# Kernel optimization log

Hardware: AMD Instinct MI355X
Metric: run time of the kernel (lower is better)

Reference implementation:

```python
import jax, jax.numpy as jnp
import numpy as np

B, S, D = 4, 2048, 1024
E = 8          # num_experts
K = 2          # top-k
H = 2048       # expert_dim


def setup_inputs() -> dict:
    key = jax.random.key(0)
    ks = jax.random.split(key, 7)
    sd = 1.0 / np.sqrt(D)
    sh = 1.0 / np.sqrt(H)
    return {
        "x": jax.random.normal(ks[0], (B, S, D), dtype=jnp.float32),
        "gate_w": jax.random.uniform(ks[1], (D, E), jnp.float32, -sd, sd),
        "gate_b": jax.random.uniform(ks[2], (E,), jnp.float32, -sd, sd),
        "w1": jax.random.uniform(ks[3], (E, D, H), jnp.float32, -sd, sd),
        "b1": jax.random.uniform(ks[4], (E, H), jnp.float32, -sd, sd),
        "w2": jax.random.uniform(ks[5], (E, H, D), jnp.float32, -sh, sh),
        "b2": jax.random.uniform(ks[6], (E, D), jnp.float32, -sh, sh),
    }


def reference(x, gate_w, gate_b, w1, b1, w2, b2):
    T = B * S
    x_flat = x.reshape(T, D)
    # gating
    gate_probs = jax.nn.softmax(x_flat @ gate_w + gate_b, axis=-1)  # [T, E]
    topw, topi = jax.lax.top_k(gate_probs, K)                        # [T, K]
    topw = topw / (jnp.sum(topw, axis=-1, keepdims=True) + 1e-9)
    # dense combine weights [T, E] (top-k indices are unique per token)
    combine = jnp.zeros((T, E), x.dtype).at[jnp.arange(T)[:, None], topi].add(topw)
    # all-experts FFN: relu(x @ W1 + b1) @ W2 + b2 per expert
    h = jax.nn.relu(jnp.einsum('td,edh->eth', x_flat, w1) + b1[:, None, :])  # [E, T, H]
    y = jnp.einsum('eth,ehd->etd', h, w2) + b2[:, None, :]                    # [E, T, D]
    out = jnp.einsum('etd,te->td', y, combine)
    return out.reshape(B, S, D)
```

## Files before the change

### kernel.cpp

```cpp
#include <hip/hip_runtime.h>
#include <hip/hip_bf16.h>
#include <math.h>

#define T_TOK 8192
#define D_DIM 1024
#define E_NUM 8
#define H_DIM 2048

typedef __bf16 bf16;
typedef __bf16 bf16x8 __attribute__((ext_vector_type(8)));
typedef __bf16 bf16x4 __attribute__((ext_vector_type(4)));
typedef float  f32x4  __attribute__((ext_vector_type(4)));

__device__ __forceinline__ void gload_lds16(const void* g, void* s) {
    __builtin_amdgcn_global_load_lds(
        (const __attribute__((address_space(1))) unsigned int*)g,
        (__attribute__((address_space(3))) unsigned int*)s, 16, 0, 0);
}

__global__ void cvt_x_kernel(const float* __restrict__ x, bf16* __restrict__ xb) {
    int i = blockIdx.x * blockDim.x + threadIdx.x;
    const float4* xp = (const float4*)x;
    float4 a = xp[i * 2];
    float4 b = xp[i * 2 + 1];
    bf16x8 o;
    o[0] = (bf16)a.x; o[1] = (bf16)a.y; o[2] = (bf16)a.z; o[3] = (bf16)a.w;
    o[4] = (bf16)b.x; o[5] = (bf16)b.y; o[6] = (bf16)b.z; o[7] = (bf16)b.w;
    *(bf16x8*)(xb + (size_t)i * 8) = o;
}

template <int K, int N>
__global__ void transpose_kernel(const float* __restrict__ W, bf16* __restrict__ Wt) {
    const int e  = blockIdx.z;
    const int kb = blockIdx.y * 32;
    const int nb = blockIdx.x * 32;
    __shared__ float tile[32][33];
    const float* We  = W  + (size_t)e * K * N;
    bf16*        Wte = Wt + (size_t)e * N * K;
    const int tid = threadIdx.x;
    const int r  = tid >> 3;
    const int c4 = (tid & 7) * 4;
    float4 v = *(const float4*)(We + (size_t)(kb + r) * N + nb + c4);
    tile[r][c4 + 0] = v.x; tile[r][c4 + 1] = v.y;
    tile[r][c4 + 2] = v.z; tile[r][c4 + 3] = v.w;
    __syncthreads();
    const int rn = tid >> 3;
    const int k4 = (tid & 7) * 4;
    bf16x4 o;
    o[0] = (bf16)tile[k4 + 0][rn]; o[1] = (bf16)tile[k4 + 1][rn];
    o[2] = (bf16)tile[k4 + 2][rn]; o[3] = (bf16)tile[k4 + 3][rn];
    *(bf16x4*)(Wte + (size_t)(nb + rn) * K + kb + k4) = o;
}

__global__ __launch_bounds__(256) void gating_kernel(
    const float* __restrict__ x, const float* __restrict__ gw,
    const float* __restrict__ gb,
    int* __restrict__ eIdx, float* __restrict__ wgt) {
    __shared__ float xs[4 * D_DIM];
    const int tid  = threadIdx.x;
    const int wave = tid >> 6;
    const int lane = tid & 63;
    {
        const float4* src = (const float4*)(x + (size_t)blockIdx.x * 4 * D_DIM);
        float4* dst = (float4*)xs;
#pragma unroll
        for (int k = 0; k < 4; k++) dst[tid + k * 256] = src[tid + k * 256];
    }
    __syncthreads();

    const int e = lane & 7;
    const int s = lane >> 3;
    const float* xw = xs + wave * D_DIM;
    double acc_a = 0.0, acc_b = 0.0;
#pragma unroll 8
    for (int i = 0; i < 128; i += 2) {
        int d0 = i * 8 + s;
        int d1 = (i + 1) * 8 + s;
        acc_a += (double)xw[d0] * (double)gw[d0 * 8 + e];
        acc_b += (double)xw[d1] * (double)gw[d1 * 8 + e];
    }
    double acc = acc_a + acc_b;
    acc += __shfl_xor(acc, 8, 64);
    acc += __shfl_xor(acc, 16, 64);
    acc += __shfl_xor(acc, 32, 64);
    double lg[E_NUM];
#pragma unroll
    for (int k = 0; k < E_NUM; k++) lg[k] = __shfl(acc, k, 64);

    if (lane == 0) {
        int token = blockIdx.x * 4 + wave;
        double v[E_NUM], p[E_NUM];
        double mx = -1e300;
#pragma unroll
        for (int k = 0; k < E_NUM; k++) { v[k] = lg[k] + (double)gb[k]; mx = fmax(mx, v[k]); }
        double sum = 0.0;
#pragma unroll
        for (int k = 0; k < E_NUM; k++) { p[k] = exp(v[k] - mx); sum += p[k]; }
        int i0 = 0; double p0 = p[0];
#pragma unroll
        for (int k = 1; k < E_NUM; k++) if (p[k] > p0) { p0 = p[k]; i0 = k; }
        int i1 = -1; double p1 = -1.0;
#pragma unroll
        for (int k = 0; k < E_NUM; k++) if (k != i0 && p[k] > p1) { p1 = p[k]; i1 = k; }
        double q0 = p0 / sum, q1 = p1 / sum;
        double sw = q0 + q1 + 1e-9;
        eIdx[token * 2]     = i0;
        eIdx[token * 2 + 1] = i1;
        wgt[token * 2]      = (float)(q0 / sw);
        wgt[token * 2 + 1]  = (float)(q1 / sw);
    }
}

__global__ void count_kernel(const int* __restrict__ eIdx, int* __restrict__ counts) {
    __shared__ int bc[E_NUM];
    const int tid = threadIdx.x;
    if (tid < E_NUM) bc[tid] = 0;
    __syncthreads();
    int2 ev = *(const int2*)(eIdx + (size_t)blockIdx.x * 512 + tid * 2);
    atomicAdd(&bc[ev.x], 1);
    atomicAdd(&bc[ev.y], 1);
    __syncthreads();
    if (tid < E_NUM) atomicAdd(&counts[tid], bc[tid]);
}

__global__ void scan_kernel(const int* __restrict__ counts, int* __restrict__ offsets) {
    if (threadIdx.x == 0) {
        int s = 0;
        for (int e = 0; e < E_NUM; e++) { offsets[e] = s; s += counts[e]; }
    }
}

__global__ void scatter_kernel(const int* __restrict__ eIdx, const int* __restrict__ offsets,
                               const float* __restrict__ wgt, int* __restrict__ fill,
                               int* __restrict__ rowIdx, float* __restrict__ wslot) {
    __shared__ int bc[E_NUM];
    __shared__ int bbase[E_NUM];
    __shared__ int bcur[E_NUM];
    const int tid = threadIdx.x;
    if (tid < E_NUM) { bc[tid] = 0; bcur[tid] = 0; }
    __syncthreads();
    int t0 = blockIdx.x * 512 + tid * 2;
    int4 ev = *(const int4*)(eIdx + (size_t)t0 * 2);
    float4 wv = *(const float4*)(wgt + (size_t)t0 * 2);
    atomicAdd(&bc[ev.x], 1);
    atomicAdd(&bc[ev.y], 1);
    atomicAdd(&bc[ev.z], 1);
    atomicAdd(&bc[ev.w], 1);
    __syncthreads();
    if (tid < E_NUM) bbase[tid] = atomicAdd(&fill[tid], bc[tid]);
    __syncthreads();
    int p0 = atomicAdd(&bcur[ev.x], 1);
    int r0 = offsets[ev.x] + bbase[ev.x] + p0;
    rowIdx[r0] = t0;     wslot[r0] = wv.x;
    int p1 = atomicAdd(&bcur[ev.y], 1);
    int r1 = offsets[ev.y] + bbase[ev.y] + p1;
    rowIdx[r1] = t0;     wslot[r1] = wv.y;
    int p2 = atomicAdd(&bcur[ev.z], 1);
    int r2 = offsets[ev.z] + bbase[ev.z] + p2;
    rowIdx[r2] = t0 + 1; wslot[r2] = wv.z;
    int p3 = atomicAdd(&bcur[ev.w], 1);
    int r3 = offsets[ev.w] + bbase[ev.w] + p3;
    rowIdx[r3] = t0 + 1; wslot[r3] = wv.w;
}

template <int KD, int ND, bool RELU, bool GATHER, bool COMBINE>
__global__ __launch_bounds__(256, 2) void moe_gemm_kernel(
    const bf16* __restrict__ A, const bf16* __restrict__ Bt,
    const float* __restrict__ bias, bf16* __restrict__ Out,
    const int* __restrict__ counts, const int* __restrict__ offsets,
    const int* __restrict__ rowIdx, const float* __restrict__ wslot,
    float* __restrict__ outF) {
    const int e  = blockIdx.z;
    const int Ne = counts[e];
    const int rb = blockIdx.y;
    if (rb * 128 >= Ne) return;
    const int base = offsets[e];
    const int n0   = blockIdx.x * 128;
    const bf16*  Be = Bt + (size_t)e * KD * ND;
    const float* be = bias + (size_t)e * ND;

    __shared__ bf16 As[128 * 64];
    __shared__ bf16 Bs[128 * 64];

    const int tid  = threadIdx.x;
    const int wave = tid >> 6;
    const int lane = tid & 63;

    const int sr = lane >> 3;
    const int cg = (lane & 7) ^ sr;
    const bf16* aP[4];
    const bf16* bP[4];
#pragma unroll
    for (int i = 0; i < 4; i++) {
        int m = rb * 128 + i * 32 + wave * 8 + sr;
        if (m >= Ne) m = Ne - 1;
        int arow = GATHER ? rowIdx[base + m] : (base + m);
        aP[i] = A + (size_t)arow * KD + cg * 8;
        int n = n0 + i * 32 + wave * 8 + sr;
        bP[i] = Be + (size_t)n * KD + cg * 8;
    }

    const int wm = (wave >> 1) * 64;
    const int wn = (wave & 1) * 64;
    const int lrow = lane & 15;
    const int quad = lane >> 4;
    const int r7   = lrow & 7;

    f32x4 acc[4][4] = {};

    for (int k0 = 0; k0 < KD; k0 += 64) {
#pragma unroll
        for (int i = 0; i < 4; i++) {
            gload_lds16(aP[i] + k0, (char*)As + i * 4096 + wave * 1024);
            gload_lds16(bP[i] + k0, (char*)Bs + i * 4096 + wave * 1024);
        }
        __syncthreads();

#pragma unroll
        for (int h = 0; h < 2; h++) {
            bf16x8 af[4], bfv[4];
#pragma unroll
            for (int t4 = 0; t4 < 4; t4++) {
                int pc = (quad + h * 4) ^ r7;
                af[t4]  = *(const bf16x8*)&As[(wm + t4 * 16 + lrow) * 64 + pc * 8];
                bfv[t4] = *(const bf16x8*)&Bs[(wn + t4 * 16 + lrow) * 64 + pc * 8];
            }
#pragma unroll
            for (int ti = 0; ti < 4; ti++)
#pragma unroll
                for (int tj = 0; tj < 4; tj++)
                    acc[ti][tj] = __builtin_amdgcn_mfma_f32_16x16x32_bf16(
                        af[ti], bfv[tj], acc[ti][tj], 0, 0, 0);
        }
        __syncthreads();
    }

    int   tokr[4][4];
    float wr[4][4];
    if (COMBINE) {
#pragma unroll
        for (int ti = 0; ti < 4; ti++)
#pragma unroll
            for (int r = 0; r < 4; r++) {
                int grow = rb * 128 + wm + ti * 16 + quad * 4 + r;
                if (grow < Ne) {
                    tokr[ti][r] = rowIdx[base + grow];
                    wr[ti][r]   = wslot[base + grow];
                }
            }
    }
#pragma unroll
    for (int ti = 0; ti < 4; ti++) {
        int rloc = wm + ti * 16 + quad * 4;
#pragma unroll
        for (int tj = 0; tj < 4; tj++) {
            int gcol = n0 + wn + tj * 16 + lrow;
            float bb = be[gcol];
#pragma unroll
            for (int r = 0; r < 4; r++) {
                int grow = rb * 128 + rloc + r;
                if (grow < Ne) {
                    float v = acc[ti][tj][r] + bb;
                    if (RELU) v = v > 0.f ? v : 0.f;
                    if (COMBINE) {
                        atomicAdd(&outF[(size_t)tokr[ti][r] * ND + gcol], v * wr[ti][r]);
                    } else {
                        Out[(size_t)(base + grow) * ND + gcol] = (bf16)v;
                    }
                }
            }
        }
    }
}

extern "C" void kernel_launch(void* const* d_in, const int* in_sizes, int n_in,
                              void* d_out, int out_size, void* d_ws, size_t ws_size,
                              hipStream_t stream) {
    const float* x  = (const float*)d_in[0];
    const float* gw = (const float*)d_in[1];
    const float* gb = (const float*)d_in[2];
    const float* w1 = (const float*)d_in[3];
    const float* b1 = (const float*)d_in[4];
    const float* w2 = (const float*)d_in[5];
    const float* b2 = (const float*)d_in[6];
    float* out = (float*)d_out;

    char* ws = (char*)d_ws;
    int*   counts = (int*)ws;
    int*   fill   = (int*)(ws + 32);
    int*   offs   = (int*)(ws + 64);
    int*   eIdx   = (int*)(ws + 256);
    float* wgt    = (float*)(ws + 65792);
    float* wslot  = (float*)(ws + 131328);
    int*   rowIdx = (int*)(ws + 196864);
    bf16*  Xb  = (bf16*)(ws + 262400);
    bf16*  Hb  = (bf16*)(ws + 17039616);
    bf16*  W2t = (bf16*)(ws + 84148480);
    bf16*  W1t = (bf16*)(ws + 117702912);

    if (ws_size < (size_t)151257344) return;

    hipMemsetAsync(ws, 0, 64, stream);
    hipMemsetAsync(out, 0, (size_t)T_TOK * D_DIM * 4, stream);
    cvt_x_kernel<<<(T_TOK * D_DIM) / (256 * 8), 256, 0, stream>>>(x, Xb);
    transpose_kernel<D_DIM, H_DIM>
        <<<dim3(H_DIM / 32, D_DIM / 32, E_NUM), 256, 0, stream>>>(w1, W1t);
    transpose_kernel<H_DIM, D_DIM>
        <<<dim3(D_DIM / 32, H_DIM / 32, E_NUM), 256, 0, stream>>>(w2, W2t);
    gating_kernel<<<T_TOK / 4, 256, 0, stream>>>(x, gw, gb, eIdx, wgt);
    count_kernel<<<T_TOK * 2 / 512, 256, 0, stream>>>(eIdx, counts);
    scan_kernel<<<1, 64, 0, stream>>>(counts, offs);
    scatter_kernel<<<T_TOK / 512, 256, 0, stream>>>(eIdx, offs, wgt, fill, rowIdx, wslot);
    moe_gemm_kernel<D_DIM, H_DIM, true, true, false>
        <<<dim3(H_DIM / 128, T_TOK / 128, E_NUM), 256, 0, stream>>>(
            Xb, W1t, b1, Hb, counts, offs, rowIdx, (const float*)nullptr, (float*)nullptr);
    moe_gemm_kernel<H_DIM, D_DIM, false, false, true>
        <<<dim3(D_DIM / 128, T_TOK / 128, E_NUM), 256, 0, stream>>>(
            Hb, W2t, b2, (bf16*)nullptr, counts, offs, rowIdx, wslot, out);
}
```

Measured before the change: 477.2 us.

## Double-buffer MoE GEMM K-loop and fuse x bf16 conversion into gating

Reworks the MoE GEMM main loop to use a 32-wide K step with two LDS buffers, so global-to-LDS loads for the next step are issued before computing on the current one and only one barrier is needed per iteration. The swizzle and loader mapping change to fit the narrower tile. It also removes the separate x-to-bf16 conversion kernel and has the gating kernel write the bf16 copy from its shared-memory tile, saving one launch and one read of x. The risks are more iterations with fewer MFMAs each and possible LDS bank conflicts from the new swizzle.

```diff
diff --git a/kernel.cpp b/kernel.cpp
--- a/kernel.cpp
+++ b/kernel.cpp
@@ -16,17 +16,6 @@
     __builtin_amdgcn_global_load_lds(
         (const __attribute__((address_space(1))) unsigned int*)g,
         (__attribute__((address_space(3))) unsigned int*)s, 16, 0, 0);
-}
-
-__global__ void cvt_x_kernel(const float* __restrict__ x, bf16* __restrict__ xb) {
-    int i = blockIdx.x * blockDim.x + threadIdx.x;
-    const float4* xp = (const float4*)x;
-    float4 a = xp[i * 2];
-    float4 b = xp[i * 2 + 1];
-    bf16x8 o;
-    o[0] = (bf16)a.x; o[1] = (bf16)a.y; o[2] = (bf16)a.z; o[3] = (bf16)a.w;
-    o[4] = (bf16)b.x; o[5] = (bf16)b.y; o[6] = (bf16)b.z; o[7] = (bf16)b.w;
-    *(bf16x8*)(xb + (size_t)i * 8) = o;
 }
 
 template <int K, int N>
@@ -55,7 +44,7 @@
 __global__ __launch_bounds__(256) void gating_kernel(
     const float* __restrict__ x, const float* __restrict__ gw,
     const float* __restrict__ gb,
-    int* __restrict__ eIdx, float* __restrict__ wgt) {
+    int* __restrict__ eIdx, float* __restrict__ wgt, bf16* __restrict__ xb) {
     __shared__ float xs[4 * D_DIM];
     const int tid  = threadIdx.x;
     const int wave = tid >> 6;
@@ -67,6 +56,17 @@
         for (int k = 0; k < 4; k++) dst[tid + k * 256] = src[tid + k * 256];
     }
     __syncthreads();
+
+    {
+        const int i0 = tid * 16;
+        bf16x8 o0, o1;
+#pragma unroll
+        for (int i = 0; i < 8; i++) o0[i] = (bf16)xs[i0 + i];
+#pragma unroll
+        for (int i = 0; i < 8; i++) o1[i] = (bf16)xs[i0 + 8 + i];
+        *(bf16x8*)(xb + (size_t)blockIdx.x * 4096 + i0)     = o0;
+        *(bf16x8*)(xb + (size_t)blockIdx.x * 4096 + i0 + 8) = o1;
+    }
 
     const int e = lane & 7;
     const int s = lane >> 3;
@@ -179,60 +179,66 @@
     const bf16*  Be = Bt + (size_t)e * KD * ND;
     const float* be = bias + (size_t)e * ND;
 
-    __shared__ bf16 As[128 * 64];
-    __shared__ bf16 Bs[128 * 64];
+    __shared__ bf16 SL[2 * 8192];
 
     const int tid  = threadIdx.x;
     const int wave = tid >> 6;
     const int lane = tid & 63;
 
-    const int sr = lane >> 3;
-    const int cg = (lane & 7) ^ sr;
-    const bf16* aP[4];
-    const bf16* bP[4];
-#pragma unroll
-    for (int i = 0; i < 4; i++) {
-        int m = rb * 128 + i * 32 + wave * 8 + sr;
+    const int srow = tid >> 2;
+    const int cg   = (tid & 3) ^ ((tid >> 3) & 3);
+    const bf16* aP[2];
+    const bf16* bP[2];
+#pragma unroll
+    for (int j = 0; j < 2; j++) {
+        int m = rb * 128 + j * 64 + srow;
         if (m >= Ne) m = Ne - 1;
         int arow = GATHER ? rowIdx[base + m] : (base + m);
-        aP[i] = A + (size_t)arow * KD + cg * 8;
-        int n = n0 + i * 32 + wave * 8 + sr;
-        bP[i] = Be + (size_t)n * KD + cg * 8;
-    }
-
-    const int wm = (wave >> 1) * 64;
-    const int wn = (wave & 1) * 64;
+        aP[j] = A + (size_t)arow * KD + cg * 8;
+        int n = n0 + j * 64 + srow;
+        bP[j] = Be + (size_t)n * KD + cg * 8;
+    }
+
+    const int wm   = (wave >> 1) * 64;
+    const int wn   = (wave & 1) * 64;
     const int lrow = lane & 15;
     const int quad = lane >> 4;
-    const int r7   = lrow & 7;
+    const int pc   = quad ^ ((lrow >> 1) & 3);
 
     f32x4 acc[4][4] = {};
 
-    for (int k0 = 0; k0 < KD; k0 += 64) {
-#pragma unroll
-        for (int i = 0; i < 4; i++) {
-            gload_lds16(aP[i] + k0, (char*)As + i * 4096 + wave * 1024);
-            gload_lds16(bP[i] + k0, (char*)Bs + i * 4096 + wave * 1024);
+    const int nit = KD / 32;
+#pragma unroll
+    for (int j = 0; j < 2; j++) {
+        gload_lds16(aP[j], (char*)SL + j * 4096 + wave * 1024);
+        gload_lds16(bP[j], (char*)SL + 8192 + j * 4096 + wave * 1024);
+    }
+    for (int it = 0; it < nit; it++) {
+        __syncthreads();
+        const int cb = it & 1;
+        if (it + 1 < nit) {
+            const int k1 = (it + 1) * 32;
+            char* dst = (char*)SL + (cb ^ 1) * 16384;
+#pragma unroll
+            for (int j = 0; j < 2; j++) {
+                gload_lds16(aP[j] + k1, dst + j * 4096 + wave * 1024);
+                gload_lds16(bP[j] + k1, dst + 8192 + j * 4096 + wave * 1024);
+            }
         }
-        __syncthreads();
-
-#pragma unroll
-        for (int h = 0; h < 2; h++) {
-            bf16x8 af[4], bfv[4];
-#pragma unroll
-            for (int t4 = 0; t4 < 4; t4++) {
-                int pc = (quad + h * 4) ^ r7;
-                af[t4]  = *(const bf16x8*)&As[(wm + t4 * 16 + lrow) * 64 + pc * 8];
-                bfv[t4] = *(const bf16x8*)&Bs[(wn + t4 * 16 + lrow) * 64 + pc * 8];
-            }
-#pragma unroll
-            for (int ti = 0; ti < 4; ti++)
-#pragma unroll
-                for (int tj = 0; tj < 4; tj++)
-                    acc[ti][tj] = __builtin_amdgcn_mfma_f32_16x16x32_bf16(
-                        af[ti], bfv[tj], acc[ti][tj], 0, 0, 0);
+        const bf16* As = SL + cb * 8192;
+        const bf16* Bs = As + 4096;
+        bf16x8 af[4], bfv[4];
+#pragma unroll
+        for (int t4 = 0; t4 < 4; t4++) {
+            af[t4]  = *(const bf16x8*)&As[(wm + t4 * 16 + lrow) * 32 + pc * 8];
+            bfv[t4] = *(const bf16x8*)&Bs[(wn + t4 * 16 + lrow) * 32 + pc * 8];
         }
-        __syncthreads();
+#pragma unroll
+        for (int ti = 0; ti < 4; ti++)
+#pragma unroll
+            for (int tj = 0; tj < 4; tj++)
+                acc[ti][tj] = __builtin_amdgcn_mfma_f32_16x16x32_bf16(
+                    af[ti], bfv[tj], acc[ti][tj], 0, 0, 0);
     }
 
     int   tokr[4][4];
@@ -302,12 +308,11 @@
 
     hipMemsetAsync(ws, 0, 64, stream);
     hipMemsetAsync(out, 0, (size_t)T_TOK * D_DIM * 4, stream);
-    cvt_x_kernel<<<(T_TOK * D_DIM) / (256 * 8), 256, 0, stream>>>(x, Xb);
     transpose_kernel<D_DIM, H_DIM>
         <<<dim3(H_DIM / 32, D_DIM / 32, E_NUM), 256, 0, stream>>>(w1, W1t);
     transpose_kernel<H_DIM, D_DIM>
         <<<dim3(D_DIM / 32, H_DIM / 32, E_NUM), 256, 0, stream>>>(w2, W2t);
-    gating_kernel<<<T_TOK / 4, 256, 0, stream>>>(x, gw, gb, eIdx, wgt);
+    gating_kernel<<<T_TOK / 4, 256, 0, stream>>>(x, gw, gb, eIdx, wgt, Xb);
     count_kernel<<<T_TOK * 2 / 512, 256, 0, stream>>>(eIdx, counts);
     scan_kernel<<<1, 64, 0, stream>>>(counts, offs);
     scatter_kernel<<<T_TOK / 512, 256, 0, stream>>>(eIdx, offs, wgt, fill, rowIdx, wslot);
```

Measured after the change: 500.5 us. 4.9% more time.
